# Kernel optimization log

Hardware: AMD Instinct MI355X
Metric: run time of the kernel (lower is better)

The kernel has to match this reference:

```python
import jax, jax.numpy as jnp
import numpy as np

B, T, C, H = 4, 2048, 1024, 16
D = C // H  # head dim = 64

def setup_inputs() -> dict:
    key = jax.random.key(0)
    k1, k2, k3, k4, k5 = jax.random.split(key, 5)
    s_in = 1.0 / np.sqrt(C)
    return {
        "inputs": jax.random.normal(k1, (B, T, C), dtype=jnp.float32),
        "W_qkv": jax.random.normal(k2, (C, 3 * C), dtype=jnp.float32) * s_in,
        "b_qkv": jnp.zeros((3 * C,), dtype=jnp.float32),
        "W_proj": jax.random.normal(k3, (C, C), dtype=jnp.float32) * s_in,
        "b_proj": jnp.zeros((C,), dtype=jnp.float32),
    }

def reference(inputs, W_qkv, b_qkv, W_proj, b_proj):
    Bq, Tq, Cq = inputs.shape
    qkv = inputs @ W_qkv + b_qkv                      # [B,T,3C]
    q, k, v = jnp.split(qkv, 3, axis=-1)              # each [B,T,C]
    # [B,T,C] -> [B,H,T,D]
    def heads(x):
        return x.reshape(Bq, Tq, H, D).transpose(0, 2, 1, 3)
    q, k, v = heads(q), heads(k), heads(v)
    scale = 1.0 / np.sqrt(D)
    att = jnp.einsum('bhqd,bhkd->bhqk', q, k) * scale  # [B,H,T,T]
    causal = jnp.tril(jnp.ones((Tq, Tq), dtype=bool))
    att = jnp.where(causal, att, -jnp.inf)
    att = jax.nn.softmax(att, axis=-1)
    out = jnp.einsum('bhqk,bhkd->bhqd', att, v)        # [B,H,T,D]
    out = out.transpose(0, 2, 1, 3).reshape(Bq, Tq, Cq)
    return out @ W_proj + b_proj
```

## Files before the change

kernel.cpp:

```cpp
#include <hip/hip_runtime.h>

typedef unsigned short u16;
typedef unsigned int u32;
typedef __attribute__((ext_vector_type(8))) short short8;
typedef __attribute__((ext_vector_type(4))) float f32x4;
typedef __attribute__((ext_vector_type(4))) float float4v;
typedef __attribute__((ext_vector_type(4))) unsigned short u16x4;

#define DEV __device__ __forceinline__

#define QSCALE 0.18033688011112042f

DEV u16 f2bf(float f) {
  u32 u = __float_as_uint(f);
  u32 r = (u + 0x7fffu + ((u >> 16) & 1u)) >> 16;
  return (u16)r;
}

DEV u32 packbf2(float lo, float hi) {
  return (u32)f2bf(lo) | ((u32)f2bf(hi) << 16);
}

DEV f32x4 mfma16(short8 a, short8 b, f32x4 c) {
  return __builtin_amdgcn_mfma_f32_16x16x32_bf16(a, b, c, 0, 0, 0);
}

DEV void gld_lds16(const void* g, void* l) {
  __builtin_amdgcn_global_load_lds(
      (const __attribute__((address_space(1))) void*)g,
      (__attribute__((address_space(3))) void*)l, 16, 0, 0);
}

__global__ void cvt_x_kernel(const float4v* __restrict__ in,
                             u16x4* __restrict__ out, int n4) {
  int i = blockIdx.x * blockDim.x + threadIdx.x;
  if (i >= n4) return;
  float4v v = in[i];
  u16x4 o;
  o.x = f2bf(v.x); o.y = f2bf(v.y); o.z = f2bf(v.z); o.w = f2bf(v.w);
  out[i] = o;
}

__global__ void cvt_w_t_kernel(const float* __restrict__ in,
                               u16* __restrict__ out, int Kd, int Nd) {
  __shared__ float tile[32][33];
  int n0 = blockIdx.x * 32, k0 = blockIdx.y * 32;
  int tx = threadIdx.x, ty = threadIdx.y;
#pragma unroll
  for (int j = 0; j < 4; ++j)
    tile[ty + 8 * j][tx] = in[(size_t)(k0 + ty + 8 * j) * Nd + n0 + tx];
  __syncthreads();
#pragma unroll
  for (int j = 0; j < 4; ++j)
    out[(size_t)(n0 + ty + 8 * j) * Kd + k0 + tx] = f2bf(tile[tx][ty + 8 * j]);
}

template <int MODE>
__global__ __launch_bounds__(256, 2) void gemm_bt(
    const u16* __restrict__ A, const u16* __restrict__ Bt,
    const float* __restrict__ bias, u16* __restrict__ q_out,
    u16* __restrict__ k_out, u16* __restrict__ vt_out,
    float* __restrict__ f_out, int M, int N, int K) {
  __shared__ u16 ldsA[128 * 64];
  __shared__ u16 ldsB[128 * 64];
  const int tid = threadIdx.x;
  const int lane = tid & 63, w = tid >> 6;
  const int g = lane >> 4, c = lane & 15;
  const int wm = w >> 1, wn = w & 1;
  const int n0 = blockIdx.x * 128, m0 = blockIdx.y * 128;

  const f32x4 fz = {0.f, 0.f, 0.f, 0.f};
  f32x4 acc[4][4];
#pragma unroll
  for (int i = 0; i < 4; ++i)
#pragma unroll
    for (int j = 0; j < 4; ++j) acc[i][j] = fz;

  const u16* Ag = A + (size_t)m0 * K;
  const u16* Bg = Bt + (size_t)n0 * K;
  const int lr = lane >> 3;
  const int kc = (lane & 7) ^ lr;

  for (int kt = 0; kt < K; kt += 64) {
#pragma unroll
    for (int qq = 0; qq < 4; ++qq) {
      int row = w * 32 + qq * 8 + lr;
      gld_lds16(Ag + (size_t)row * K + kt + kc * 8, &ldsA[(w * 32 + qq * 8) * 64]);
      gld_lds16(Bg + (size_t)row * K + kt + kc * 8, &ldsB[(w * 32 + qq * 8) * 64]);
    }
    __syncthreads();
#pragma unroll
    for (int ks = 0; ks < 2; ++ks) {
      short8 ar[4], br[4];
#pragma unroll
      for (int mr = 0; mr < 4; ++mr) {
        int row = wm * 64 + mr * 16 + c;
        ar[mr] = *(const short8*)&ldsA[row * 64 + (((ks * 4 + g) ^ (row & 7)) << 3)];
      }
#pragma unroll
      for (int nf = 0; nf < 4; ++nf) {
        int row = wn * 64 + nf * 16 + c;
        br[nf] = *(const short8*)&ldsB[row * 64 + (((ks * 4 + g) ^ (row & 7)) << 3)];
      }
#pragma unroll
      for (int mr = 0; mr < 4; ++mr)
#pragma unroll
        for (int nf = 0; nf < 4; ++nf)
          acc[mr][nf] = mfma16(ar[mr], br[nf], acc[mr][nf]);
    }
    __syncthreads();
  }

#pragma unroll
  for (int mr = 0; mr < 4; ++mr) {
#pragma unroll
    for (int nf = 0; nf < 4; ++nf) {
#pragma unroll
      for (int r = 0; r < 4; ++r) {
        int gm = m0 + wm * 64 + mr * 16 + 4 * g + r;
        int gn = n0 + wn * 64 + nf * 16 + c;
        float val = acc[mr][nf][r] + bias[gn];
        if (MODE == 0) {
          int sec = gn >> 10, cc = gn & 1023;
          int hh = cc >> 6, dd = cc & 63;
          int bb = gm >> 11, tt = gm & 2047;
          if (sec == 0)
            q_out[((size_t)(bb * 16 + hh) * 2048 + tt) * 64 + dd] =
                f2bf(val * QSCALE);
          else if (sec == 1)
            k_out[((size_t)(bb * 16 + hh) * 2048 + tt) * 64 + dd] = f2bf(val);
          else
            vt_out[((size_t)(bb * 16 + hh) * 64 + dd) * 2048 + tt] = f2bf(val);
        } else {
          f_out[(size_t)gm * N + gn] = val;
        }
      }
    }
  }
}

__global__ __launch_bounds__(256, 4) void attn_fwd(
    const u16* __restrict__ Qb, const u16* __restrict__ Kb,
    const u16* __restrict__ VTb, u16* __restrict__ Ob) {
  __shared__ u16 lds[2][8192];
  const int lane = threadIdx.x & 63, w = threadIdx.x >> 6;
  const int g = lane >> 4, c = lane & 15;
  const int bi = blockIdx.x;
  const int bh = ((bi & 7) << 3) | ((bi >> 3) & 7);
  const int qblock = 31 - (bi >> 6);
  const int b = bh >> 4, h = bh & 15;
  const size_t base = (size_t)bh * (2048 * 64);
  const u16* Qp = Qb + base;
  const u16* Kp = Kb + base;
  const u16* VTp = VTb + base;

  const int qw = qblock * 64 + w * 16;
  const int qg = qw + c;
  const int nt = qblock + 1;

  short8 qf0 = *(const short8*)&Qp[(qw + c) * 64 + g * 8];
  short8 qf1 = *(const short8*)&Qp[(qw + c) * 64 + 32 + g * 8];

  const f32x4 fz = {0.f, 0.f, 0.f, 0.f};
  f32x4 o[4];
#pragma unroll
  for (int d0 = 0; d0 < 4; ++d0) o[d0] = fz;
  float m = -1e30f, lsum = 0.f;

  const int srow = lane >> 3;
  const int sgx = (lane & 7) ^ (srow & 7);
  auto stage = [&](int t, int buf) {
#pragma unroll
    for (int q = 0; q < 4; ++q) {
      const int i = w * 4 + q;
      const int row = ((i & 7) << 3) | srow;
      const int k0 = t << 6;
      const u16* src = (i < 8)
          ? Kp + (size_t)(k0 + row) * 64 + sgx * 8
          : VTp + (size_t)row * 2048 + k0 + sgx * 8;
      gld_lds16(src, &lds[buf][i * 512]);
    }
  };

  stage(0, 0);
  __syncthreads();

  for (int t = 0; t < nt; ++t) {
    const int cur = t & 1;
    if (t + 1 < nt) stage(t + 1, cur ^ 1);
    const u16* Kl = &lds[cur][0];
    const u16* Vl = &lds[cur][4096];
    const int k0b = t << 6;
    const int cx = c & 7;

    float pv[16];
#pragma unroll
    for (int j = 0; j < 4; ++j) {
      short8 ka = *(const short8*)&Kl[(16 * j + c) * 64 + ((g ^ cx) << 3)];
      short8 kb = *(const short8*)&Kl[(16 * j + c) * 64 + (((4 + g) ^ cx) << 3)];
      f32x4 s = mfma16(ka, qf0, fz);
      s = mfma16(kb, qf1, s);
#pragma unroll
      for (int r = 0; r < 4; ++r) pv[j * 4 + r] = s[r];
    }

    if (t == nt - 1) {
#pragma unroll
      for (int j = 0; j < 4; ++j)
#pragma unroll
        for (int r = 0; r < 4; ++r)
          if (k0b + 16 * j + 4 * g + r > qg) pv[j * 4 + r] = -1e30f;
    }

    float mx[8];
#pragma unroll
    for (int i = 0; i < 8; ++i) mx[i] = fmaxf(pv[2 * i], pv[2 * i + 1]);
#pragma unroll
    for (int i = 0; i < 4; ++i) mx[i] = fmaxf(mx[i], mx[i + 4]);
    float tm = fmaxf(fmaxf(mx[0], mx[1]), fmaxf(mx[2], mx[3]));
    tm = fmaxf(tm, __shfl_xor(tm, 16));
    tm = fmaxf(tm, __shfl_xor(tm, 32));
    float mn = fmaxf(m, tm);
    float sc = __builtin_amdgcn_exp2f(m - mn);
    m = mn;
#pragma unroll
    for (int i = 0; i < 16; ++i) pv[i] = __builtin_amdgcn_exp2f(pv[i] - mn);
    float sx[8];
#pragma unroll
    for (int i = 0; i < 8; ++i) sx[i] = pv[2 * i] + pv[2 * i + 1];
#pragma unroll
    for (int i = 0; i < 4; ++i) sx[i] = sx[i] + sx[i + 4];
    float rs = (sx[0] + sx[1]) + (sx[2] + sx[3]);
    rs += __shfl_xor(rs, 16);
    rs += __shfl_xor(rs, 32);
    lsum = lsum * sc + rs;
#pragma unroll
    for (int d0 = 0; d0 < 4; ++d0)
#pragma unroll
      for (int r = 0; r < 4; ++r) o[d0][r] *= sc;

    u32 P2[8];
#pragma unroll
    for (int j = 0; j < 4; ++j) {
      P2[j * 2 + 0] = packbf2(pv[j * 4 + 0], pv[j * 4 + 1]);
      P2[j * 2 + 1] = packbf2(pv[j * 4 + 2], pv[j * 4 + 3]);
    }

#pragma unroll
    for (int hh = 0; hh < 2; ++hh) {
      u32 pbw[4];
#pragma unroll
      for (int i = 0; i < 4; ++i) {
        int src = c + ((2 * (g & 1) + (i >> 1)) << 4);
        int a0 = __shfl((int)P2[(2 * hh) * 2 + (i & 1)], src);
        int a1 = __shfl((int)P2[(2 * hh + 1) * 2 + (i & 1)], src);
        pbw[i] = (g < 2) ? (u32)a0 : (u32)a1;
      }
      short8 pb = *(short8*)pbw;
#pragma unroll
      for (int d0 = 0; d0 < 4; ++d0) {
        short8 va = *(const short8*)
            &Vl[(d0 * 16 + c) * 64 + (((4 * hh + g) ^ cx) << 3)];
        o[d0] = mfma16(va, pb, o[d0]);
      }
    }
    __syncthreads();
  }

  float inv = 1.f / lsum;
  u16* Op = Ob + (size_t)(b * 2048 + qw + c) * 1024 + h * 64;
#pragma unroll
  for (int d0 = 0; d0 < 4; ++d0) {
    u16x4 wv;
#pragma unroll
    for (int r = 0; r < 4; ++r) wv[r] = f2bf(o[d0][r] * inv);
    *(u16x4*)(Op + d0 * 16 + 4 * g) = wv;
  }
}

extern "C" void kernel_launch(void* const* d_in, const int* in_sizes, int n_in,
                              void* d_out, int out_size, void* d_ws,
                              size_t ws_size, hipStream_t stream) {
  (void)in_sizes; (void)n_in; (void)out_size; (void)ws_size;
  const float* X = (const float*)d_in[0];
  const float* Wqkv = (const float*)d_in[1];
  const float* bqkv = (const float*)d_in[2];
  const float* Wproj = (const float*)d_in[3];
  const float* bproj = (const float*)d_in[4];
  float* out = (float*)d_out;

  char* ws = (char*)d_ws;
  u16* Xb = (u16*)ws;
  u16* WqkvT = (u16*)(ws + (16u << 20));
  u16* WprojT = (u16*)(ws + (22u << 20));
  u16* Qb = (u16*)(ws + (24u << 20));
  u16* Kb = (u16*)(ws + (40u << 20));
  u16* VT = (u16*)(ws + (56u << 20));

  cvt_x_kernel<<<dim3(8192), dim3(256), 0, stream>>>(
      (const float4v*)X, (u16x4*)Xb, 8192 * 1024 / 4);
  cvt_w_t_kernel<<<dim3(96, 32), dim3(32, 8), 0, stream>>>(Wqkv, WqkvT, 1024, 3072);
  cvt_w_t_kernel<<<dim3(32, 32), dim3(32, 8), 0, stream>>>(Wproj, WprojT, 1024, 1024);

  gemm_bt<0><<<dim3(24, 64), dim3(256), 0, stream>>>(
      Xb, WqkvT, bqkv, Qb, Kb, VT, (float*)nullptr, 8192, 3072, 1024);

  attn_fwd<<<dim3(2048), dim3(256), 0, stream>>>(Qb, Kb, VT, Xb);

  gemm_bt<1><<<dim3(8, 64), dim3(256), 0, stream>>>(
      Xb, WprojT, bproj, (u16*)nullptr, (u16*)nullptr, (u16*)nullptr, out,
      8192, 1024, 1024);
}
```

Baseline: 291.9 us.

## Add hardware bf16 pack, XCD-aware GEMM tile swizzle, lazy softmax rescale

Replaces the software bf16 rounding with the v_cvt_pk_bf16_f32 instruction in the conversion, attention and epilogue paths. GEMM blocks are remapped with a 1D grid so consecutive tiles land on the same XCD, aiming at better L2 reuse. Attention now rescales the running max and accumulators only when some lane's new max exceeds the old one by more than 8 (log2 units), skipping most exp and multiply work. It also raises the occupancy hint to 5 and vectorises the V-transpose stores. The lazy rescale lets unnormalised values grow up to 2^8 before rescaling, and the hardware pack may round differently from the old code.

```diff
diff --git a/kernel.cpp b/kernel.cpp
--- a/kernel.cpp
+++ b/kernel.cpp
@@ -6,6 +6,7 @@
 typedef __attribute__((ext_vector_type(4))) float f32x4;
 typedef __attribute__((ext_vector_type(4))) float float4v;
 typedef __attribute__((ext_vector_type(4))) unsigned short u16x4;
+typedef __attribute__((ext_vector_type(2))) u32 u32x2;
 
 #define DEV __device__ __forceinline__
 
@@ -17,8 +18,10 @@
   return (u16)r;
 }
 
-DEV u32 packbf2(float lo, float hi) {
-  return (u32)f2bf(lo) | ((u32)f2bf(hi) << 16);
+DEV u32 cvtpk(float lo, float hi) {
+  u32 r;
+  asm("v_cvt_pk_bf16_f32 %0, %1, %2" : "=v"(r) : "v"(lo), "v"(hi));
+  return r;
 }
 
 DEV f32x4 mfma16(short8 a, short8 b, f32x4 c) {
@@ -32,12 +35,13 @@
 }
 
 __global__ void cvt_x_kernel(const float4v* __restrict__ in,
-                             u16x4* __restrict__ out, int n4) {
+                             u32x2* __restrict__ out, int n4) {
   int i = blockIdx.x * blockDim.x + threadIdx.x;
   if (i >= n4) return;
   float4v v = in[i];
-  u16x4 o;
-  o.x = f2bf(v.x); o.y = f2bf(v.y); o.z = f2bf(v.z); o.w = f2bf(v.w);
+  u32x2 o;
+  o.x = cvtpk(v.x, v.y);
+  o.y = cvtpk(v.z, v.w);
   out[i] = o;
 }
 
@@ -67,7 +71,15 @@
   const int lane = tid & 63, w = tid >> 6;
   const int g = lane >> 4, c = lane & 15;
   const int wm = w >> 1, wn = w & 1;
-  const int n0 = blockIdx.x * 128, m0 = blockIdx.y * 128;
+
+  const int total = gridDim.x;
+  const int cpx = total >> 3;
+  const int wg = blockIdx.x;
+  const int swz = (wg & 7) * cpx + (wg >> 3);
+  const int mtiles = M >> 7;
+  const int by = swz & (mtiles - 1);
+  const int bx = swz / mtiles;
+  const int n0 = bx * 128, m0 = by * 128;
 
   const f32x4 fz = {0.f, 0.f, 0.f, 0.f};
   f32x4 acc[4][4];
@@ -115,31 +127,41 @@
   for (int mr = 0; mr < 4; ++mr) {
 #pragma unroll
     for (int nf = 0; nf < 4; ++nf) {
-#pragma unroll
-      for (int r = 0; r < 4; ++r) {
-        int gm = m0 + wm * 64 + mr * 16 + 4 * g + r;
-        int gn = n0 + wn * 64 + nf * 16 + c;
-        float val = acc[mr][nf][r] + bias[gn];
-        if (MODE == 0) {
-          int sec = gn >> 10, cc = gn & 1023;
-          int hh = cc >> 6, dd = cc & 63;
-          int bb = gm >> 11, tt = gm & 2047;
-          if (sec == 0)
-            q_out[((size_t)(bb * 16 + hh) * 2048 + tt) * 64 + dd] =
-                f2bf(val * QSCALE);
-          else if (sec == 1)
-            k_out[((size_t)(bb * 16 + hh) * 2048 + tt) * 64 + dd] = f2bf(val);
-          else
-            vt_out[((size_t)(bb * 16 + hh) * 64 + dd) * 2048 + tt] = f2bf(val);
+      const int gm0 = m0 + wm * 64 + mr * 16 + 4 * g;
+      const int gn = n0 + wn * 64 + nf * 16 + c;
+      float v4[4];
+#pragma unroll
+      for (int r = 0; r < 4; ++r) v4[r] = acc[mr][nf][r] + bias[gn];
+      if (MODE == 0) {
+        const int sec = gn >> 10, cc = gn & 1023;
+        const int hh = cc >> 6, dd = cc & 63;
+        const int bb = gm0 >> 11, tt0 = gm0 & 2047;
+        if (sec == 0) {
+#pragma unroll
+          for (int r = 0; r < 4; ++r)
+            q_out[((size_t)(bb * 16 + hh) * 2048 + tt0 + r) * 64 + dd] =
+                f2bf(v4[r] * QSCALE);
+        } else if (sec == 1) {
+#pragma unroll
+          for (int r = 0; r < 4; ++r)
+            k_out[((size_t)(bb * 16 + hh) * 2048 + tt0 + r) * 64 + dd] =
+                f2bf(v4[r]);
         } else {
-          f_out[(size_t)gm * N + gn] = val;
+          u32x2 pkd;
+          pkd.x = cvtpk(v4[0], v4[1]);
+          pkd.y = cvtpk(v4[2], v4[3]);
+          *(u32x2*)&vt_out[((size_t)(bb * 16 + hh) * 64 + dd) * 2048 + tt0] = pkd;
         }
+      } else {
+#pragma unroll
+        for (int r = 0; r < 4; ++r)
+          f_out[(size_t)(gm0 + r) * N + gn] = v4[r];
       }
     }
   }
 }
 
-__global__ __launch_bounds__(256, 4) void attn_fwd(
+__global__ __launch_bounds__(256, 5) void attn_fwd(
     const u16* __restrict__ Qb, const u16* __restrict__ Kb,
     const u16* __restrict__ VTb, u16* __restrict__ Ob) {
   __shared__ u16 lds[2][8192];
@@ -220,11 +242,20 @@
     float tm = fmaxf(fmaxf(mx[0], mx[1]), fmaxf(mx[2], mx[3]));
     tm = fmaxf(tm, __shfl_xor(tm, 16));
     tm = fmaxf(tm, __shfl_xor(tm, 32));
-    float mn = fmaxf(m, tm);
-    float sc = __builtin_amdgcn_exp2f(m - mn);
-    m = mn;
-#pragma unroll
-    for (int i = 0; i < 16; ++i) pv[i] = __builtin_amdgcn_exp2f(pv[i] - mn);
+
+    if (__any(tm > m + 8.f)) {
+      float mn = fmaxf(m, tm);
+      float sc = __builtin_amdgcn_exp2f(m - mn);
+      m = mn;
+      lsum *= sc;
+#pragma unroll
+      for (int d0 = 0; d0 < 4; ++d0)
+#pragma unroll
+        for (int r = 0; r < 4; ++r) o[d0][r] *= sc;
+    }
+
+#pragma unroll
+    for (int i = 0; i < 16; ++i) pv[i] = __builtin_amdgcn_exp2f(pv[i] - m);
     float sx[8];
 #pragma unroll
     for (int i = 0; i < 8; ++i) sx[i] = pv[2 * i] + pv[2 * i + 1];
@@ -233,17 +264,13 @@
     float rs = (sx[0] + sx[1]) + (sx[2] + sx[3]);
     rs += __shfl_xor(rs, 16);
     rs += __shfl_xor(rs, 32);
-    lsum = lsum * sc + rs;
-#pragma unroll
-    for (int d0 = 0; d0 < 4; ++d0)
-#pragma unroll
-      for (int r = 0; r < 4; ++r) o[d0][r] *= sc;
+    lsum += rs;
 
     u32 P2[8];
 #pragma unroll
     for (int j = 0; j < 4; ++j) {
-      P2[j * 2 + 0] = packbf2(pv[j * 4 + 0], pv[j * 4 + 1]);
-      P2[j * 2 + 1] = packbf2(pv[j * 4 + 2], pv[j * 4 + 3]);
+      P2[j * 2 + 0] = cvtpk(pv[j * 4 + 0], pv[j * 4 + 1]);
+      P2[j * 2 + 1] = cvtpk(pv[j * 4 + 2], pv[j * 4 + 3]);
     }
 
 #pragma unroll
@@ -271,10 +298,10 @@
   u16* Op = Ob + (size_t)(b * 2048 + qw + c) * 1024 + h * 64;
 #pragma unroll
   for (int d0 = 0; d0 < 4; ++d0) {
-    u16x4 wv;
-#pragma unroll
-    for (int r = 0; r < 4; ++r) wv[r] = f2bf(o[d0][r] * inv);
-    *(u16x4*)(Op + d0 * 16 + 4 * g) = wv;
+    u32x2 pk;
+    pk.x = cvtpk(o[d0][0] * inv, o[d0][1] * inv);
+    pk.y = cvtpk(o[d0][2] * inv, o[d0][3] * inv);
+    *(u32x2*)(Op + d0 * 16 + 4 * g) = pk;
   }
 }
 
@@ -298,16 +325,16 @@
   u16* VT = (u16*)(ws + (56u << 20));
 
   cvt_x_kernel<<<dim3(8192), dim3(256), 0, stream>>>(
-      (const float4v*)X, (u16x4*)Xb, 8192 * 1024 / 4);
+      (const float4v*)X, (u32x2*)Xb, 8192 * 1024 / 4);
   cvt_w_t_kernel<<<dim3(96, 32), dim3(32, 8), 0, stream>>>(Wqkv, WqkvT, 1024, 3072);
   cvt_w_t_kernel<<<dim3(32, 32), dim3(32, 8), 0, stream>>>(Wproj, WprojT, 1024, 1024);
 
-  gemm_bt<0><<<dim3(24, 64), dim3(256), 0, stream>>>(
+  gemm_bt<0><<<dim3(1536), dim3(256), 0, stream>>>(
       Xb, WqkvT, bqkv, Qb, Kb, VT, (float*)nullptr, 8192, 3072, 1024);
 
   attn_fwd<<<dim3(2048), dim3(256), 0, stream>>>(Qb, Kb, VT, Xb);
 
-  gemm_bt<1><<<dim3(8, 64), dim3(256), 0, stream>>>(
+  gemm_bt<1><<<dim3(512), dim3(256), 0, stream>>>(
       Xb, WprojT, bproj, (u16*)nullptr, (u16*)nullptr, (u16*)nullptr, out,
       8192, 1024, 1024);
 }
```

Measured after the change: 276.8 us. -5.1%, faster.
